# Optimization experiments

Hardware: AMD Instinct MI355X
Metric: run time of the kernel (lower is better)

The kernel has to match this reference:

```python
import jax, jax.numpy as jnp
import numpy as np

# NFFT config (matches torch NFFT(N=(256,256), m=4, sigma=2.0))
N = (256, 256)          # output Fourier grid
n = (512, 512)          # oversampled grid (2*(int(sigma*N)//2))
m = 4                   # window half-width -> (2m)^2 = 64 taps per point
B, C, M = 2, 2, 200000  # batch, channels, nonuniform points
SIGMA = tuple(n[i] / N[i] for i in range(2))  # KaiserBesselWindow sigma = n/N


def kb_phi(k):
    """Kaiser-Bessel window phi(k), k: (..., 2). Matches KaiserBesselWindow.forward."""
    nv = jnp.asarray(n, dtype=k.dtype)
    b = (2.0 - 1.0 / jnp.asarray(SIGMA, dtype=k.dtype)) * jnp.pi
    t = m * m - (nv * k) ** 2
    safe = t > 0
    arg = jnp.sqrt(jnp.where(safe, t, 1.0))
    out = jnp.where(safe, jnp.sinh(b * arg) / (arg * jnp.pi), 0.0)  # nan_to_num(...,0) equiv.
    return jnp.prod(out, axis=-1)


def kb_phi_hat():
    """Fourier coefficients of the window on the N-grid (KaiserBesselWindow.ft)."""
    grids = jnp.meshgrid(*[jnp.arange(-(N[i] // 2), N[i] // 2, dtype=jnp.float32)
                           for i in range(2)], indexing='ij')
    inds = jnp.stack(grids, axis=-1)                                 # (N1,N2,2)
    nv = jnp.asarray(n, jnp.float32)
    b = (2.0 - 1.0 / jnp.asarray(SIGMA, jnp.float32)) * jnp.pi
    ft = jnp.i0(m * jnp.sqrt(b ** 2 - (2.0 * jnp.pi * inds / nv) ** 2))
    return jnp.prod(ft, axis=-1)                                     # (N1,N2)


def setup_inputs() -> dict:
    key = jax.random.key(0)
    k1, k2, k3 = jax.random.split(key, 3)
    x = jax.random.uniform(k1, (B, 1, M, 2), dtype=jnp.float32) - 0.5  # points in [-1/2,1/2)
    f_hat_real = jax.random.normal(k2, (B, C, N[0], N[1]), dtype=jnp.float32)
    f_hat_imag = jax.random.normal(k3, (B, C, N[0], N[1]), dtype=jnp.float32)
    return {"x": x, "f_hat_real": f_hat_real, "f_hat_imag": f_hat_imag}


def reference(x, f_hat_real, f_hat_imag):
    f_hat = f_hat_real + 1j * f_hat_imag                              # (B,C,N1,N2) complex64
    # deconvolve by window Fourier coefficients
    g_hat = f_hat / kb_phi_hat()
    # zero-pad to oversampled grid n
    cut = [(n[i] - N[i]) // 2 for i in range(2)]
    g_hat = jnp.pad(g_hat, ((0, 0), (0, 0), (cut[0], cut[0]), (cut[1], cut[1])))
    ax = (-2, -1)
    g = jnp.fft.ifftshift(jnp.fft.fft2(jnp.fft.fftshift(g_hat, ax), norm='backward'), ax)
    # windowed gather (sparse_convolution): (2m)^2 taps per nonuniform point
    r = jnp.arange(2 * m, dtype=jnp.int32)
    off = jnp.stack(jnp.meshgrid(r, r, indexing='ij'), axis=-1).reshape(-1, 2)  # (64,2)
    nv = jnp.asarray(n, jnp.float32)
    base = jnp.ceil(x * nv).astype(jnp.int32) - m                     # (B,1,M,2)
    inds = base[None] + off[:, None, None, None, :]                   # (64,B,1,M,2)
    w = kb_phi(x[None] - inds.astype(jnp.float32) / nv)               # (64,B,1,M)
    half = jnp.asarray([n[0] // 2, n[1] // 2], jnp.int32)
    nn = jnp.asarray(n, jnp.int32)
    im = (inds + half) % nn                                           # wrap onto grid
    g2 = jnp.transpose(g, (0, 2, 3, 1))                               # (B,n1,n2,C)
    bidx = jnp.arange(B, dtype=jnp.int32)[None, :, None, None]
    gl = g2[bidx, im[..., 0], im[..., 1]]                             # (64,B,1,M,C)
    f = jnp.sum(gl * w[..., None].astype(gl.dtype), axis=0)           # (B,1,M,C)
    return jnp.transpose(f[:, 0], (0, 2, 1))                          # (B,C,M) complex64
```

## Files before the change

### kernel.cpp

```cpp
#include <hip/hip_runtime.h>
#include <math.h>


#define NGRID 512
#define NSMALL 256
#define MW 4
#define BB 2
#define CC 2
#define MPTS 200000
#define PLANE (BB * CC * MPTS)
#define LPAD4 513
#define IMG4 (NGRID * NGRID)
#define G16OFF(b) ((size_t)(b) * 524288 + 131072)

__device__ __forceinline__ float nfft29781_i0_large(float z) {
    float inv = 1.0f / z;
    float p = 1.0f + inv * (0.125f + inv * (0.0703125f
              + inv * (0.0732421875f + inv * 0.112152099609375f)));
    return expf(z) * rsqrtf(2.0f * (float)M_PI * z) * p;
}

__device__ __forceinline__ int nfft29781_brev9(int v) {
    return (int)(__brev((unsigned)v) >> 23);
}

__device__ __forceinline__ unsigned nfft29781_bf16pack(float a, float b) {
    unsigned ua = __float_as_uint(a);
    ua += 0x7FFFu + ((ua >> 16) & 1u);
    unsigned ub = __float_as_uint(b);
    ub += 0x7FFFu + ((ub >> 16) & 1u);
    return (ua >> 16) | (ub & 0xFFFF0000u);
}

__device__ __forceinline__ void nfft29781_fft512_c2(float4* s, int tid) {
    #pragma unroll
    for (int st = 0; st < 9; ++st) {
        int half = 1 << st;
        int pos = tid & (half - 1);
        int i0 = ((tid >> st) << (st + 1)) + pos;
        int i1 = i0 + half;
        float ang = -(float)M_PI * (float)pos / (float)half;
        float sn, cs;
        __sincosf(ang, &sn, &cs);
        float4 a = s[i0];
        float4 b = s[i1];
        float4 tw;
        tw.x = b.x * cs - b.y * sn;  tw.y = b.x * sn + b.y * cs;
        tw.z = b.z * cs - b.w * sn;  tw.w = b.z * sn + b.w * cs;
        s[i0] = make_float4(a.x + tw.x, a.y + tw.y, a.z + tw.z, a.w + tw.w);
        s[i1] = make_float4(a.x - tw.x, a.y - tw.y, a.z - tw.z, a.w - tw.w);
        __syncthreads();
    }
}

__global__ __launch_bounds__(256) void nfft29781_rows2(const float* __restrict__ fr,
                                                       const float* __restrict__ fi,
                                                       float4* __restrict__ G32) {
    __shared__ float4 s[NGRID];
    int tid = threadIdx.x;
    int b   = blockIdx.x >> 8;
    int a1  = blockIdx.x & 255;

    const float bcon  = 1.5f * (float)M_PI;
    const float scale = 2.0f * (float)M_PI / (float)NGRID;
    float k1 = (float)(a1 - 128) * scale;
    float p1 = nfft29781_i0_large((float)MW * sqrtf(bcon * bcon - k1 * k1));

    int a2 = tid ^ 128;
    float k2 = (float)(a2 - 128) * scale;
    float p2 = nfft29781_i0_large((float)MW * sqrtf(bcon * bcon - k2 * k2));
    float invp = 1.0f / (p1 * p2);

    size_t s0 = ((size_t)(b * CC + 0) * NSMALL + a1) * NSMALL + a2;
    size_t s1 = ((size_t)(b * CC + 1) * NSMALL + a1) * NSMALL + a2;
    float4 v = make_float4(fr[s0] * invp, fi[s0] * invp,
                           fr[s1] * invp, fi[s1] * invp);

    int j2v = (tid < 128) ? tid : tid + 256;
    int j2z = (tid < 128) ? tid + 256 : tid;
    s[nfft29781_brev9(j2v)] = v;
    s[nfft29781_brev9(j2z)] = make_float4(0.0f, 0.0f, 0.0f, 0.0f);
    __syncthreads();

    nfft29781_fft512_c2(s, tid);

    int j1 = (a1 < 128) ? a1 + 384 : a1 - 128;
    float4* Gb = G32 + (size_t)b * IMG4 + (size_t)j1 * NGRID;
    Gb[tid]       = s[tid];
    Gb[tid + 256] = s[tid + 256];
}

__global__ __launch_bounds__(256) void nfft29781_cols2(float4* __restrict__ G32) {
    __shared__ float4 s[4 * LPAD4];
    int tid  = threadIdx.x;
    int b    = blockIdx.x >> 7;
    int col0 = (blockIdx.x & 127) << 2;
    const float4* Gb = G32 + (size_t)b * IMG4;

    #pragma unroll
    for (int it = 0; it < 4; ++it) {
        int e  = it * 256 + tid;
        int cp = e & 3;
        int q  = e >> 2;
        int r  = (q < 128) ? q : q + 256;
        s[cp * LPAD4 + nfft29781_brev9(r)] = Gb[(size_t)r * NGRID + col0 + cp];
    }
    #pragma unroll
    for (int it = 0; it < 4; ++it) {
        int e  = it * 256 + tid;
        int cp = e & 3;
        int q  = e >> 2;
        s[cp * LPAD4 + nfft29781_brev9(q + 128)] = make_float4(0.0f, 0.0f, 0.0f, 0.0f);
    }
    __syncthreads();

    int c = tid & 3;
    int w = tid >> 2;
    float4* sc = s + c * LPAD4;
    for (int st = 0; st < 9; ++st) {
        int half = 1 << st;
        #pragma unroll
        for (int k = 0; k < 4; ++k) {
            int bf  = w + (k << 6);
            int pos = bf & (half - 1);
            int i0  = ((bf >> st) << (st + 1)) + pos;
            int i1  = i0 + half;
            float ang = -(float)M_PI * (float)pos / (float)half;
            float sn, cs;
            __sincosf(ang, &sn, &cs);
            float4 a = sc[i0];
            float4 bb = sc[i1];
            float4 tw;
            tw.x = bb.x * cs - bb.y * sn;  tw.y = bb.x * sn + bb.y * cs;
            tw.z = bb.z * cs - bb.w * sn;  tw.w = bb.z * sn + bb.w * cs;
            sc[i0] = make_float4(a.x + tw.x, a.y + tw.y, a.z + tw.z, a.w + tw.w);
            sc[i1] = make_float4(a.x - tw.x, a.y - tw.y, a.z - tw.z, a.w - tw.w);
        }
        __syncthreads();
    }

    uint2* G16 = (uint2*)G32 + G16OFF(b);
    #pragma unroll
    for (int it = 0; it < 8; ++it) {
        int e  = it * 256 + tid;
        int cp = e & 3;
        int r  = e >> 2;
        float4 v = s[cp * LPAD4 + r];
        uint2 pk;
        pk.x = nfft29781_bf16pack(v.x, v.y);
        pk.y = nfft29781_bf16pack(v.z, v.w);
        G16[(size_t)r * NGRID + col0 + cp] = pk;
    }
}

__global__ __launch_bounds__(256) void nfft29781_gather_bf16(const float* __restrict__ x,
                                                             const uint2* __restrict__ G16base,
                                                             float* __restrict__ out,
                                                             int out_elems) {
    int t  = blockIdx.x * blockDim.x + threadIdx.x;
    int j  = t & 7;
    int pp = t >> 3;
    if (pp >= BB * MPTS) return;
    int b  = (pp >= MPTS) ? 1 : 0;
    int pt = pp - b * MPTS;

    float u0 = x[(size_t)pp * 2 + 0] * (float)NGRID;
    float u1 = x[(size_t)pp * 2 + 1] * (float)NGRID;

    float c0 = ceilf(u0), c1 = ceilf(u1);
    int base0 = (int)c0 - MW;
    int base1 = (int)c1 - MW;
    float d0 = c0 - u0, d1 = c1 - u1;

    const float bw = 1.5f * (float)M_PI;
    const float invpi = 1.0f / (float)M_PI;
    float w0m, w1m;
    {
        float nk = (float)(MW - j) - d0;
        float tt = (float)(MW * MW) - nk * nk;
        w0m = 0.0f;
        if (tt > 0.0f) { float a = sqrtf(tt); float e = expf(bw * a);
                         w0m = (e - 1.0f / e) * 0.5f * invpi / a; }
        nk = (float)(MW - j) - d1;
        tt = (float)(MW * MW) - nk * nk;
        w1m = 0.0f;
        if (tt > 0.0f) { float a = sqrtf(tt); float e = expf(bw * a);
                         w1m = (e - 1.0f / e) * 0.5f * invpi / a; }
    }

    const uint2* Gi = G16base + G16OFF(b);
    int cix = (base1 + j) & (NGRID - 1);
    int lanebase = (threadIdx.x & 63) & ~7;

    float a0x = 0.0f, a0y = 0.0f, a1x = 0.0f, a1y = 0.0f;
    #pragma unroll
    for (int i = 0; i < 8; ++i) {
        float w0i = __shfl(w0m, lanebase + i, 64);
        uint2 g = Gi[(size_t)(((base0 + i) & (NGRID - 1)) << 9) + cix];
        float g0x = __uint_as_float(g.x << 16);
        float g0y = __uint_as_float(g.x & 0xFFFF0000u);
        float g1x = __uint_as_float(g.y << 16);
        float g1y = __uint_as_float(g.y & 0xFFFF0000u);
        a0x += w0i * g0x;  a0y += w0i * g0y;
        a1x += w0i * g1x;  a1y += w0i * g1y;
    }
    a0x *= w1m;  a0y *= w1m;  a1x *= w1m;  a1y *= w1m;

    #pragma unroll
    for (int msk = 1; msk < 8; msk <<= 1) {
        a0x += __shfl_xor(a0x, msk, 64);
        a0y += __shfl_xor(a0y, msk, 64);
        a1x += __shfl_xor(a1x, msk, 64);
        a1y += __shfl_xor(a1y, msk, 64);
    }

    if (j == 0) {
        size_t o0 = (size_t)(b * CC) * MPTS + pt;
        size_t o1 = o0 + MPTS;
        if (o0 < (size_t)out_elems)         out[o0]         = a0x;
        if (PLANE + o0 < (size_t)out_elems) out[PLANE + o0] = a0y;
        if (o1 < (size_t)out_elems)         out[o1]         = a1x;
        if (PLANE + o1 < (size_t)out_elems) out[PLANE + o1] = a1y;
    }
}

extern "C" void kernel_launch(void* const* d_in, const int* in_sizes, int n_in,
                              void* d_out, int out_size, void* d_ws, size_t ws_size,
                              hipStream_t stream) {
    (void)in_sizes; (void)n_in;
    const float* x  = (const float*)d_in[0];
    const float* fr = (const float*)d_in[1];
    const float* fi = (const float*)d_in[2];
    float*  out = (float*)d_out;
    float4* G32 = (float4*)d_ws;

    const size_t fullBytes = (size_t)BB * IMG4 * sizeof(float4);
    if (ws_size < fullBytes) return;

    nfft29781_rows2<<<BB * NSMALL, 256, 0, stream>>>(fr, fi, G32);
    nfft29781_cols2<<<BB * (NGRID / 4), 256, 0, stream>>>(G32);
    int gthreads = BB * MPTS * 8;
    nfft29781_gather_bf16<<<(gthreads + 255) / 256, 256, 0, stream>>>(
        x, (const uint2*)d_ws, out, out_size);
}
```

Baseline: 99.20 us.

## Fold zero-padded first FFT stage, hoist twiddles, use fast intrinsics

```diff
diff --git a/kernel.cpp b/kernel.cpp
--- a/kernel.cpp
+++ b/kernel.cpp
@@ -14,10 +14,10 @@
 #define G16OFF(b) ((size_t)(b) * 524288 + 131072)
 
 __device__ __forceinline__ float nfft29781_i0_large(float z) {
-    float inv = 1.0f / z;
+    float inv = __builtin_amdgcn_rcpf(z);
     float p = 1.0f + inv * (0.125f + inv * (0.0703125f
               + inv * (0.0732421875f + inv * 0.112152099609375f)));
-    return expf(z) * rsqrtf(2.0f * (float)M_PI * z) * p;
+    return __expf(z) * rsqrtf(2.0f * (float)M_PI * z) * p;
 }
 
 __device__ __forceinline__ int nfft29781_brev9(int v) {
@@ -30,27 +30,6 @@
     unsigned ub = __float_as_uint(b);
     ub += 0x7FFFu + ((ub >> 16) & 1u);
     return (ua >> 16) | (ub & 0xFFFF0000u);
-}
-
-__device__ __forceinline__ void nfft29781_fft512_c2(float4* s, int tid) {
-    #pragma unroll
-    for (int st = 0; st < 9; ++st) {
-        int half = 1 << st;
-        int pos = tid & (half - 1);
-        int i0 = ((tid >> st) << (st + 1)) + pos;
-        int i1 = i0 + half;
-        float ang = -(float)M_PI * (float)pos / (float)half;
-        float sn, cs;
-        __sincosf(ang, &sn, &cs);
-        float4 a = s[i0];
-        float4 b = s[i1];
-        float4 tw;
-        tw.x = b.x * cs - b.y * sn;  tw.y = b.x * sn + b.y * cs;
-        tw.z = b.z * cs - b.w * sn;  tw.w = b.z * sn + b.w * cs;
-        s[i0] = make_float4(a.x + tw.x, a.y + tw.y, a.z + tw.z, a.w + tw.w);
-        s[i1] = make_float4(a.x - tw.x, a.y - tw.y, a.z - tw.z, a.w - tw.w);
-        __syncthreads();
-    }
 }
 
 __global__ __launch_bounds__(256) void nfft29781_rows2(const float* __restrict__ fr,
@@ -69,7 +48,7 @@
     int a2 = tid ^ 128;
     float k2 = (float)(a2 - 128) * scale;
     float p2 = nfft29781_i0_large((float)MW * sqrtf(bcon * bcon - k2 * k2));
-    float invp = 1.0f / (p1 * p2);
+    float invp = __builtin_amdgcn_rcpf(p1 * p2);
 
     size_t s0 = ((size_t)(b * CC + 0) * NSMALL + a1) * NSMALL + a2;
     size_t s1 = ((size_t)(b * CC + 1) * NSMALL + a1) * NSMALL + a2;
@@ -77,12 +56,35 @@
                            fr[s1] * invp, fi[s1] * invp);
 
     int j2v = (tid < 128) ? tid : tid + 256;
-    int j2z = (tid < 128) ? tid + 256 : tid;
-    s[nfft29781_brev9(j2v)] = v;
-    s[nfft29781_brev9(j2z)] = make_float4(0.0f, 0.0f, 0.0f, 0.0f);
+    int pidx = nfft29781_brev9(j2v);
+    int pe = pidx & ~1;
+    s[pe]     = v;
+    s[pe + 1] = (pidx & 1) ? make_float4(-v.x, -v.y, -v.z, -v.w) : v;
     __syncthreads();
 
-    nfft29781_fft512_c2(s, tid);
+    #pragma unroll
+    for (int st = 1; st < 9; ++st) {
+        int half = 1 << st;
+        int pos = tid & (half - 1);
+        int i0 = ((tid >> st) << (st + 1)) + pos;
+        int i1 = i0 + half;
+        float sn, cs;
+        if (st == 1) {
+            cs = pos ? 0.0f : 1.0f;
+            sn = pos ? -1.0f : 0.0f;
+        } else {
+            float ang = -(float)M_PI * (float)pos / (float)half;
+            __sincosf(ang, &sn, &cs);
+        }
+        float4 a = s[i0];
+        float4 bq = s[i1];
+        float4 tw;
+        tw.x = bq.x * cs - bq.y * sn;  tw.y = bq.x * sn + bq.y * cs;
+        tw.z = bq.z * cs - bq.w * sn;  tw.w = bq.z * sn + bq.w * cs;
+        s[i0] = make_float4(a.x + tw.x, a.y + tw.y, a.z + tw.z, a.w + tw.w);
+        s[i1] = make_float4(a.x - tw.x, a.y - tw.y, a.z - tw.z, a.w - tw.w);
+        __syncthreads();
+    }
 
     int j1 = (a1 < 128) ? a1 + 384 : a1 - 128;
     float4* Gb = G32 + (size_t)b * IMG4 + (size_t)j1 * NGRID;
@@ -103,31 +105,58 @@
         int cp = e & 3;
         int q  = e >> 2;
         int r  = (q < 128) ? q : q + 256;
-        s[cp * LPAD4 + nfft29781_brev9(r)] = Gb[(size_t)r * NGRID + col0 + cp];
-    }
-    #pragma unroll
-    for (int it = 0; it < 4; ++it) {
-        int e  = it * 256 + tid;
-        int cp = e & 3;
-        int q  = e >> 2;
-        s[cp * LPAD4 + nfft29781_brev9(q + 128)] = make_float4(0.0f, 0.0f, 0.0f, 0.0f);
+        float4 v = Gb[(size_t)r * NGRID + col0 + cp];
+        int pidx = nfft29781_brev9(r);
+        int pe = pidx & ~1;
+        float4* scw = s + cp * LPAD4;
+        scw[pe]     = v;
+        scw[pe + 1] = (pidx & 1) ? make_float4(-v.x, -v.y, -v.z, -v.w) : v;
     }
     __syncthreads();
 
     int c = tid & 3;
     int w = tid >> 2;
     float4* sc = s + c * LPAD4;
-    for (int st = 0; st < 9; ++st) {
-        int half = 1 << st;
+    #pragma unroll
+    for (int st = 1; st < 9; ++st) {
+        const int half = 1 << st;
+        float csk[4], snk[4];
+        if (st <= 6) {
+            int pos = w & (half - 1);
+            float sn, cs;
+            if (st == 1) {
+                cs = pos ? 0.0f : 1.0f;
+                sn = pos ? -1.0f : 0.0f;
+            } else {
+                float ang = -(float)M_PI * (float)pos / (float)half;
+                __sincosf(ang, &sn, &cs);
+            }
+            csk[0] = csk[1] = csk[2] = csk[3] = cs;
+            snk[0] = snk[1] = snk[2] = snk[3] = sn;
+        } else if (st == 7) {
+            #pragma unroll
+            for (int k = 0; k < 2; ++k) {
+                int pos = (w + (k << 6)) & 127;
+                float ang = -(float)M_PI * (float)pos / 128.0f;
+                __sincosf(ang, &snk[k], &csk[k]);
+            }
+            csk[2] = csk[0]; snk[2] = snk[0];
+            csk[3] = csk[1]; snk[3] = snk[1];
+        } else {
+            #pragma unroll
+            for (int k = 0; k < 4; ++k) {
+                int pos = w + (k << 6);
+                float ang = -(float)M_PI * (float)pos / 256.0f;
+                __sincosf(ang, &snk[k], &csk[k]);
+            }
+        }
         #pragma unroll
         for (int k = 0; k < 4; ++k) {
             int bf  = w + (k << 6);
             int pos = bf & (half - 1);
             int i0  = ((bf >> st) << (st + 1)) + pos;
             int i1  = i0 + half;
-            float ang = -(float)M_PI * (float)pos / (float)half;
-            float sn, cs;
-            __sincosf(ang, &sn, &cs);
+            float cs = csk[k], sn = snk[k];
             float4 a = sc[i0];
             float4 bb = sc[i1];
             float4 tw;
@@ -179,13 +208,21 @@
         float nk = (float)(MW - j) - d0;
         float tt = (float)(MW * MW) - nk * nk;
         w0m = 0.0f;
-        if (tt > 0.0f) { float a = sqrtf(tt); float e = expf(bw * a);
-                         w0m = (e - 1.0f / e) * 0.5f * invpi / a; }
+        if (tt > 0.0f) {
+            float ra = __builtin_amdgcn_rsqf(tt);
+            float a  = tt * ra;
+            float e  = __expf(bw * a);
+            w0m = (e - __builtin_amdgcn_rcpf(e)) * (0.5f * invpi) * ra;
+        }
         nk = (float)(MW - j) - d1;
         tt = (float)(MW * MW) - nk * nk;
         w1m = 0.0f;
-        if (tt > 0.0f) { float a = sqrtf(tt); float e = expf(bw * a);
-                         w1m = (e - 1.0f / e) * 0.5f * invpi / a; }
+        if (tt > 0.0f) {
+            float ra = __builtin_amdgcn_rsqf(tt);
+            float a  = tt * ra;
+            float e  = __expf(bw * a);
+            w1m = (e - __builtin_amdgcn_rcpf(e)) * (0.5f * invpi) * ra;
+        }
     }
 
     const uint2* Gi = G16base + G16OFF(b);
```

New measurement: 95.05 us (median of 2 runs). 1.04x faster.
